# Kernel tuning notes

Hardware: AMD Instinct MI355X
Metric: run time of the kernel (lower is better)

The kernel has to match this reference:

```python
import jax, jax.numpy as jnp
import numpy as np
from jax import lax

MIN_R = 0.01
RADIUS = 0.8
NSAMPLE = 32
PRED_NSAMPLE = 16
TEMPERATURE = 1.0
DIV_COEF = 10.0
GRID3 = 64  # grid_size**3, grid_size=4
EPS = 1e-5


def _ball_query(q, xyz, radius, nsample):
    """q (M,3), xyz (N,3), radius scalar or (M,). Returns idx (M,nsample) int32, empty (M,) bool.
    Mirrors stack ball_query CUDA op: first-found neighbors within radius, padded with first index."""
    N = xyz.shape[0]
    d2 = jnp.sum((q[:, None, :] - xyz[None, :, :]) ** 2, axis=-1)  # (M,N)
    r = jnp.broadcast_to(jnp.asarray(radius, d2.dtype), (q.shape[0],))[:, None]
    valid = d2 < r * r
    score = jnp.where(valid, -jnp.arange(N, dtype=jnp.int32), -(N + 1))
    vals, _ = lax.top_k(score, nsample)  # largest score == smallest valid index
    idx = -vals
    pad = idx == (N + 1)
    idx = jnp.where(pad, idx[:, :1], idx)  # pad with first found neighbor
    empty = pad[:, 0]                       # no neighbor at all
    idx = jnp.where(empty[:, None], 0, idx)
    return idx, empty


def _group(q, xyz, feats, idx, empty):
    """QueryAndGroup gather: relative xyz concat point features; zero empty queries.
    Returns (M, nsample, 3+C)."""
    g_xyz = xyz[idx] - q[:, None, :]
    g = jnp.concatenate([g_xyz, feats[idx]], axis=-1)
    return jnp.where(empty[:, None, None], jnp.zeros((), g.dtype), g)


def _mlp(x, params):
    """Shared 1x1 Conv2d + BatchNorm2d(training stats) + ReLU stack. x: (B,M,S,C)."""
    for W, g, b in params:
        x = jnp.einsum('bmsc,cd->bmsd', x, W)
        mu = x.mean(axis=(0, 1, 2))
        var = x.var(axis=(0, 1, 2))
        x = (x - mu) * lax.rsqrt(var + EPS) * g + b
        x = jax.nn.relu(x)
    return x


def setup_inputs() -> dict:
    key = jax.random.key(0)
    ks = jax.random.split(key, 16)
    B, N, C, R, Croi = 2, 8192, 32, 64, 128
    scene = jnp.array([10.0, 10.0, 4.0], jnp.float32)
    xyz = jax.random.uniform(ks[0], (B, N, 3), jnp.float32) * scene
    features = jax.random.normal(ks[1], (B, N, C), jnp.float32)
    rois = jax.random.uniform(ks[2], (B, R, GRID3, 3), jnp.float32) * scene
    roi_features = jax.random.normal(ks[3], (B, R, Croi), jnp.float32)

    def kaiming(k, fi, fo):
        return jax.random.normal(k, (fi, fo), jnp.float32) * np.float32(np.sqrt(2.0 / fi))

    return {
        'xyz': xyz, 'features': features, 'rois': rois, 'roi_features': roi_features,
        'temperature_decay': jnp.ones((1,), jnp.float32),
        # predict mlp: [32+3, 32, 32]
        'pw0': kaiming(ks[4], 35, 32), 'pg0': jnp.ones(32), 'pb0': jnp.zeros(32),
        'pw1': kaiming(ks[5], 32, 32), 'pg1': jnp.ones(32), 'pb1': jnp.zeros(32),
        # feat mlp: [32+3, 64, 64]
        'fw0': kaiming(ks[6], 35, 64), 'fg0': jnp.ones(64), 'fb0': jnp.zeros(64),
        'fw1': kaiming(ks[7], 64, 64), 'fg1': jnp.ones(64), 'fb1': jnp.zeros(64),
        # predict fc: [32*64 + 128, 1]
        'fcw': kaiming(ks[8], 2176, 1), 'fcb': jnp.zeros(1),
    }


def reference(xyz, features, rois, roi_features, temperature_decay,
              pw0, pg0, pb0, pw1, pg1, pb1,
              fw0, fg0, fb0, fw1, fg1, fb1, fcw, fcb):
    B, num_rois = rois.shape[0], rois.shape[1]
    new_xyz = rois.reshape(B, -1, 3)  # (B, M, 3), M = num_rois*grid^3

    # ---- radius-prediction branch: fixed-radius grouping + MLP + max-pool ----
    idx_p, empty_p = jax.vmap(lambda q, x: _ball_query(q, x, RADIUS, PRED_NSAMPLE))(new_xyz, xyz)
    gp = jax.vmap(_group)(new_xyz, xyz, features, idx_p, empty_p)  # (B,M,S,3+C)
    gp = _mlp(gp, [(pw0, pg0, pb0), (pw1, pg1, pb1)])
    pooled = gp.max(axis=2)                       # (B, M, Cp)
    pooled = pooled.reshape(B, num_rois, -1)      # (B, R, grid^3*Cp)
    res = jnp.concatenate([pooled, roi_features], axis=-1) @ fcw + fcb  # (B,R,1)
    r = jnp.maximum(res / DIV_COEF + RADIUS, MIN_R)
    r_pts = jnp.broadcast_to(r, (B, num_rois, GRID3)).reshape(B, -1)    # (B, M)

    # ---- deformable branch: per-query radius grouping + soft weights ----
    idx_d, empty_d = jax.vmap(lambda q, x, rr: _ball_query(q, x, rr, NSAMPLE))(new_xyz, xyz, r_pts)
    gd = jax.vmap(_group)(new_xyz, xyz, features, idx_d, empty_d)       # (B,M,S,3+C)
    dist = jnp.linalg.norm(gd[..., :3], axis=-1)                        # (B,M,S)
    w = jax.nn.sigmoid((r_pts[..., None] - dist) / (TEMPERATURE * temperature_decay[0]))
    w = jnp.where(empty_d[..., None], jnp.zeros((), w.dtype), w)
    gd = _mlp(gd, [(fw0, fg0, fb0), (fw1, fg1, fb1)])                   # (B,M,S,Cout)
    new_feats = (w[..., None] * gd).max(axis=2)                          # (B,M,Cout)

    return new_xyz.reshape(-1, 3), new_feats.reshape(-1, new_feats.shape[-1])
```

## Files before the change

### kernel.cpp

```cpp
#include <hip/hip_runtime.h>
#include <hip/hip_fp16.h>

#define NB 2
#define NPTS 8192
#define NQ 4096
#define MTOT 8192
#define SP 16
#define SD 32
#define CIN 32
#define CP 32
#define CF 64
#define NROI 128
#define RADIUS_C 0.8f
#define MIN_R_C 0.01f
#define DIV_COEF_C 10.0f
#define TILE 512

__device__ int   g_idx_p[MTOT * SP];
__device__ int   g_empty_p[MTOT];
__device__ int   g_idx_d[MTOT * SD];
__device__ int   g_empty_d[MTOT];
__device__ unsigned char g_xa[(size_t)MTOT * SD * CF * 2];
__device__ unsigned char g_xb[(size_t)MTOT * SD * CF * 2];
__device__ float g_psT[CF * 2048];
__device__ float g_pqT[CF * 2048];
__device__ float g_bnscale[4][CF];
__device__ float g_bnshift[4][CF];
__device__ float g_pdot[MTOT];
__device__ float g_rroi[NROI];

__global__ void copy_xyz_kernel(const float* __restrict__ rois, float* __restrict__ out) {
    int i = blockIdx.x * 256 + threadIdx.x;
    if (i < MTOT * 3) out[i] = rois[i];
}

template <int NS>
__launch_bounds__(256, 8)
__global__ void bq_kernel(const float* __restrict__ xyz, const float* __restrict__ newxyz) {
    __shared__ float4 l4[TILE * 3 / 4];
    __shared__ int s_active;
    int tid = threadIdx.x;
    int wave = tid >> 6, lane = tid & 63;
    int q = blockIdx.x * 4 + wave;
    int b = q >> 12;
    const float4* xb4 = (const float4*)(xyz + (size_t)b * NPTS * 3);
    const float* lp = (const float*)l4;
    float qx = newxyz[q * 3 + 0], qy = newxyz[q * 3 + 1], qz = newxyz[q * 3 + 2];
    float r = (NS == SP) ? RADIUS_C : g_rroi[q >> 6];
    float r2 = r * r;
    int* idx_out   = (NS == SP) ? g_idx_p   : g_idx_d;
    int* empty_out = (NS == SP) ? g_empty_p : g_empty_d;

    int cnt = 0, first_idx = 0;
    for (int t = 0; t < NPTS / TILE; ++t) {
        l4[tid] = xb4[t * 384 + tid];
        if (tid + 256 < 384) l4[tid + 256] = xb4[t * 384 + tid + 256];
        if (tid == 0) s_active = 0;
        __syncthreads();
        if (cnt < NS) {
            for (int s = 0; s < TILE / 64; ++s) {
                int pl = s * 64 + lane;
                float dx = qx - lp[3 * pl + 0];
                float dy = qy - lp[3 * pl + 1];
                float dz = qz - lp[3 * pl + 2];
                bool valid = (dx * dx + dy * dy + dz * dz) < r2;
                unsigned long long mask = __ballot(valid);
                if (cnt == 0 && mask) first_idx = t * TILE + s * 64 + (int)__builtin_ctzll(mask);
                int pos = cnt + __popcll(mask & ((1ull << lane) - 1ull));
                if (valid && pos < NS) idx_out[q * NS + pos] = t * TILE + s * 64 + lane;
                cnt += __popcll(mask);
                if (cnt >= NS) break;
            }
            if (cnt < NS && lane == 0) s_active = 1;
        }
        __syncthreads();
        if (!s_active) break;
    }
    if (cnt == 0) {
        if (lane < NS) idx_out[q * NS + lane] = 0;
        if (lane == 0) empty_out[q] = 1;
    } else {
        int filled = cnt < NS ? cnt : NS;
        if (lane >= filled && lane < NS) idx_out[q * NS + lane] = first_idx;
        if (lane == 0) empty_out[q] = 0;
    }
}

template <int NS, int CH, bool HALF>
__launch_bounds__(128, 4)
__global__ void mlp_passA_kernel(const float* __restrict__ xyz, const float* __restrict__ feats,
                                 const float* __restrict__ newxyz, const float* __restrict__ W0,
                                 void* __restrict__ xout_) {
    constexpr int GSTR = 37;
    constexpr int SST  = CH + 2;
    __shared__ float buf[128 * GSTR];
    __shared__ float ls[128], lq[128];
    int tid = threadIdx.x;
    int rowbase = blockIdx.x * 128;
    int row = rowbase + tid;
    int q = row / NS, b = q >> 12;
    const int* idx_arr = (NS == SP) ? g_idx_p : g_idx_d;
    const int* emp_arr = (NS == SP) ? g_empty_p : g_empty_d;
    {
        float* dst = &buf[tid * GSTR];
        if (emp_arr[q]) {
#pragma unroll
            for (int c = 0; c < 35; ++c) dst[c] = 0.f;
        } else {
            int idx = idx_arr[row];
            const float* xp = xyz + (size_t)b * NPTS * 3 + idx * 3;
            dst[0] = xp[0] - newxyz[q * 3 + 0];
            dst[1] = xp[1] - newxyz[q * 3 + 1];
            dst[2] = xp[2] - newxyz[q * 3 + 2];
            const float4* fp = (const float4*)(feats + (size_t)b * NPTS * CIN + (size_t)idx * CIN);
#pragma unroll
            for (int j = 0; j < 8; ++j) {
                float4 v = fp[j];
                dst[3 + 4 * j + 0] = v.x; dst[3 + 4 * j + 1] = v.y;
                dst[3 + 4 * j + 2] = v.z; dst[3 + 4 * j + 3] = v.w;
            }
        }
    }
    float acc[CH];
#pragma unroll
    for (int ch = 0; ch < CH; ++ch) acc[ch] = 0.f;
    {
        const float* inrow = &buf[tid * GSTR];
        for (int c = 0; c < 35; ++c) {
            float h = inrow[c];
#pragma unroll
            for (int ch = 0; ch < CH; ++ch) acc[ch] = fmaf(h, W0[c * CH + ch], acc[ch]);
        }
    }
    float* xf = (float*)xout_;
    __half* xh = (__half*)xout_;
    float sum = 0.f, sq = 0.f;
#pragma unroll
    for (int p = 0; p < 2; ++p) {
        __syncthreads();
        if ((tid >> 6) == p) {
            float* srow = &buf[(tid & 63) * SST];
#pragma unroll
            for (int ch = 0; ch < CH; ++ch) srow[ch] = acc[ch];
        }
        __syncthreads();
        if (CH == 64) {
            int ch = tid & 63, rg = tid >> 6;
            for (int r = 0; r < 32; ++r) {
                float v = buf[(rg * 32 + r) * SST + ch];
                size_t o = (size_t)(rowbase + p * 64 + rg * 32 + r) * CH + ch;
                if (HALF) xh[o] = __float2half_rn(v); else xf[o] = v;
                sum += v; sq += v * v;
            }
        } else {
            int ch = tid & 31, rg = tid >> 5;
            for (int r = 0; r < 16; ++r) {
                float v = buf[(rg * 16 + r) * SST + ch];
                size_t o = (size_t)(rowbase + p * 64 + rg * 16 + r) * CH + ch;
                if (HALF) xh[o] = __float2half_rn(v); else xf[o] = v;
                sum += v; sq += v * v;
            }
        }
    }
    ls[tid] = sum; lq[tid] = sq;
    __syncthreads();
    if (CH == 64) {
        if (tid < 64) {
            g_psT[tid * 2048 + blockIdx.x] = ls[tid] + ls[64 + tid];
            g_pqT[tid * 2048 + blockIdx.x] = lq[tid] + lq[64 + tid];
        }
    } else {
        if (tid < 32) {
            g_psT[tid * 2048 + blockIdx.x] = ls[tid] + ls[32 + tid] + ls[64 + tid] + ls[96 + tid];
            g_pqT[tid * 2048 + blockIdx.x] = lq[tid] + lq[32 + tid] + lq[64 + tid] + lq[96 + tid];
        }
    }
}

template <int NS, int CH>
__launch_bounds__(128, 4)
__global__ void mlp_passB_kernel(const float* __restrict__ W1, const float* __restrict__ xin,
                                 float* __restrict__ xout, int bn0) {
    constexpr int HSTR = 33;
    constexpr int SST  = CH + 2;
    __shared__ float buf[128 * 37];
    __shared__ float ls[128], lq[128];
    int tid = threadIdx.x;
    int rowbase = blockIdx.x * 128;
    const float* sc0 = g_bnscale[bn0];
    const float* sh0 = g_bnshift[bn0];
    float acc2[CH];
#pragma unroll
    for (int ch = 0; ch < CH; ++ch) acc2[ch] = 0.f;
    const float4* src = (const float4*)xin;
#pragma unroll
    for (int hc = 0; hc < CH / 32; ++hc) {
        if (hc) __syncthreads();
#pragma unroll
        for (int k = 0; k < 8; ++k) {
            int o4 = tid + k * 128;
            int rloc = o4 >> 3, j = o4 & 7;
            int c = 4 * j, gc = hc * 32 + c;
            float4 v = src[(size_t)(rowbase + rloc) * (CH / 4) + hc * 8 + j];
            float* d = &buf[rloc * HSTR + c];
            d[0] = fmaxf(fmaf(v.x, sc0[gc + 0], sh0[gc + 0]), 0.f);
            d[1] = fmaxf(fmaf(v.y, sc0[gc + 1], sh0[gc + 1]), 0.f);
            d[2] = fmaxf(fmaf(v.z, sc0[gc + 2], sh0[gc + 2]), 0.f);
            d[3] = fmaxf(fmaf(v.w, sc0[gc + 3], sh0[gc + 3]), 0.f);
        }
        __syncthreads();
        const float* hrow = &buf[tid * HSTR];
        for (int c = 0; c < 32; ++c) {
            float h = hrow[c];
#pragma unroll
            for (int ch = 0; ch < CH; ++ch)
                acc2[ch] = fmaf(h, W1[(hc * 32 + c) * CH + ch], acc2[ch]);
        }
    }
    float sum = 0.f, sq = 0.f;
#pragma unroll
    for (int p = 0; p < 2; ++p) {
        __syncthreads();
        if ((tid >> 6) == p) {
            float* srow = &buf[(tid & 63) * SST];
#pragma unroll
            for (int ch = 0; ch < CH; ++ch) srow[ch] = acc2[ch];
        }
        __syncthreads();
        int ch = tid & 31, rg = tid >> 5;
        for (int r = 0; r < 16; ++r) {
            float v = buf[(rg * 16 + r) * SST + ch];
            xout[(size_t)(rowbase + p * 64 + rg * 16 + r) * CH + ch] = v;
            sum += v; sq += v * v;
        }
    }
    ls[tid] = sum; lq[tid] = sq;
    __syncthreads();
    if (tid < 32) {
        g_psT[tid * 2048 + blockIdx.x] = ls[tid] + ls[32 + tid] + ls[64 + tid] + ls[96 + tid];
        g_pqT[tid * 2048 + blockIdx.x] = lq[tid] + lq[32 + tid] + lq[64 + tid] + lq[96 + tid];
    }
}

__launch_bounds__(128, 4)
__global__ void mlp_fB_kernel(const float* __restrict__ W1, const __half* __restrict__ xin,
                              __half* __restrict__ xout) {
    __shared__ float fbuf[64 * 66];
    __shared__ float ls[128], lq[128];
    __half* hbuf = (__half*)fbuf;
    unsigned int* w32 = (unsigned int*)fbuf;
    int tid = threadIdx.x;
    int rowbase = blockIdx.x * 128;
    {
        const float4* src = (const float4*)xin;
#pragma unroll
        for (int k = 0; k < 8; ++k) {
            int o4 = tid + k * 128;
            int rloc = o4 >> 3, j = o4 & 7;
            float4 v = src[(size_t)(rowbase + rloc) * 8 + j];
            const unsigned int* s32 = (const unsigned int*)&v;
#pragma unroll
            for (int m = 0; m < 4; ++m) w32[rloc * 33 + 4 * j + m] = s32[m];
        }
    }
    __syncthreads();
    const float* sc0 = g_bnscale[2];
    const float* sh0 = g_bnshift[2];
    float acc2[CF];
#pragma unroll
    for (int ch = 0; ch < CF; ++ch) acc2[ch] = 0.f;
    {
        const __half* hrow = &hbuf[tid * 66];
        for (int c = 0; c < 64; ++c) {
            float h = fmaxf(fmaf(__half2float(hrow[c]), sc0[c], sh0[c]), 0.f);
#pragma unroll
            for (int ch = 0; ch < CF; ++ch)
                acc2[ch] = fmaf(h, W1[c * CF + ch], acc2[ch]);
        }
    }
    float sum = 0.f, sq = 0.f;
#pragma unroll
    for (int p = 0; p < 2; ++p) {
        __syncthreads();
        if ((tid >> 6) == p) {
            float* srow = &fbuf[(tid & 63) * 66];
#pragma unroll
            for (int ch = 0; ch < CF; ++ch) srow[ch] = acc2[ch];
        }
        __syncthreads();
        int ch = tid & 63, rg = tid >> 6;
        for (int r = 0; r < 32; ++r) {
            float v = fbuf[(rg * 32 + r) * 66 + ch];
            xout[(size_t)(rowbase + p * 64 + rg * 32 + r) * CF + ch] = __float2half_rn(v);
            sum += v; sq += v * v;
        }
    }
    ls[tid] = sum; lq[tid] = sq;
    __syncthreads();
    if (tid < 64) {
        g_psT[tid * 2048 + blockIdx.x] = ls[tid] + ls[64 + tid];
        g_pqT[tid * 2048 + blockIdx.x] = lq[tid] + lq[64 + tid];
    }
}

__global__ void passC_f_kernel(const float* __restrict__ xyz, const float* __restrict__ newxyz,
                               const float* __restrict__ td, const __half* __restrict__ xin,
                               float* __restrict__ out) {
    __shared__ float lw[64];
    int tid = threadIdx.x;
    int qpair = blockIdx.x * 2;
    if (tid < 64) {
        int ql = tid >> 5, s = tid & 31;
        int q = qpair + ql;
        float wv = 0.f;
        if (!g_empty_d[q]) {
            int idx = g_idx_d[q * SD + s];
            int b = q >> 12;
            float dx = xyz[(size_t)b * NPTS * 3 + idx * 3 + 0] - newxyz[q * 3 + 0];
            float dy = xyz[(size_t)b * NPTS * 3 + idx * 3 + 1] - newxyz[q * 3 + 1];
            float dz = xyz[(size_t)b * NPTS * 3 + idx * 3 + 2] - newxyz[q * 3 + 2];
            float dist = sqrtf(dx * dx + dy * dy + dz * dz);
            float rq = g_rroi[q >> 6];
            wv = 1.f / (1.f + expf(-(rq - dist) / td[0]));
        }
        lw[tid] = wv;
    }
    __syncthreads();
    int ql = tid >> 6, ch = tid & 63;
    int q = qpair + ql;
    float sc = g_bnscale[3][ch], sh = g_bnshift[3][ch];
    float m = 0.f;
    for (int s = 0; s < SD; ++s) {
        float v = __half2float(xin[((size_t)q * SD + s) * CF + ch]);
        m = fmaxf(m, lw[ql * 32 + s] * fmaxf(fmaf(v, sc, sh), 0.f));
    }
    out[MTOT * 3 + (size_t)q * CF + ch] = m;
}

__global__ void passC_p_kernel(const float* __restrict__ fcw, const float* __restrict__ xin) {
    int tid = threadIdx.x;
    int q = blockIdx.x * 8 + (tid >> 5);
    int ch = tid & 31;
    float sc = g_bnscale[1][ch], sh = g_bnshift[1][ch];
    float m = 0.f;
    for (int s = 0; s < SP; ++s) {
        float v = xin[(size_t)(q * SP + s) * CP + ch] * sc + sh;
        m = fmaxf(m, fmaxf(v, 0.f));
    }
    float pd = m * fcw[(q & 63) * CP + ch];
    for (int off = 16; off > 0; off >>= 1) pd += __shfl_down(pd, off, 32);
    if (ch == 0) g_pdot[q] = pd;
}

__global__ void finalize_kernel(const float* __restrict__ gamma, const float* __restrict__ beta,
                                float n, int layer, int nblocks) {
    __shared__ double l_s[256], l_q[256];
    int ch = blockIdx.x, tid = threadIdx.x;
    double s = 0, q = 0;
    for (int i = tid; i < nblocks; i += 256) { s += g_psT[ch * 2048 + i]; q += g_pqT[ch * 2048 + i]; }
    l_s[tid] = s; l_q[tid] = q; __syncthreads();
    for (int off = 128; off > 0; off >>= 1) {
        if (tid < off) { l_s[tid] += l_s[tid + off]; l_q[tid] += l_q[tid + off]; }
        __syncthreads();
    }
    if (tid == 0) {
        double mu = l_s[0] / (double)n;
        double var = l_q[0] / (double)n - mu * mu;
        if (var < 0) var = 0;
        double sc = (double)gamma[ch] / sqrt(var + 1e-5);
        g_bnscale[layer][ch] = (float)sc;
        g_bnshift[layer][ch] = (float)((double)beta[ch] - mu * sc);
    }
}

__global__ void roi_r_kernel(const float* __restrict__ roif, const float* __restrict__ fcw,
                             const float* __restrict__ fcb) {
    int tid = threadIdx.x;
    int roi = blockIdx.x * 4 + (tid >> 6);
    int lane = tid & 63;
    float acc = g_pdot[roi * 64 + lane]
              + roif[roi * 128 + lane]      * fcw[2048 + lane]
              + roif[roi * 128 + 64 + lane] * fcw[2048 + 64 + lane];
    for (int off = 32; off > 0; off >>= 1) acc += __shfl_down(acc, off, 64);
    if (lane == 0) {
        float res = acc + fcb[0];
        g_rroi[roi] = fmaxf(res / DIV_COEF_C + RADIUS_C, MIN_R_C);
    }
}

extern "C" void kernel_launch(void* const* d_in, const int* in_sizes, int n_in,
                              void* d_out, int out_size, void* d_ws, size_t ws_size,
                              hipStream_t stream) {
    const float* xyz   = (const float*)d_in[0];
    const float* feats = (const float*)d_in[1];
    const float* rois  = (const float*)d_in[2];
    const float* roif  = (const float*)d_in[3];
    const float* td    = (const float*)d_in[4];
    const float* pw0 = (const float*)d_in[5];
    const float* pg0 = (const float*)d_in[6];
    const float* pb0 = (const float*)d_in[7];
    const float* pw1 = (const float*)d_in[8];
    const float* pg1 = (const float*)d_in[9];
    const float* pb1 = (const float*)d_in[10];
    const float* fw0 = (const float*)d_in[11];
    const float* fg0 = (const float*)d_in[12];
    const float* fb0 = (const float*)d_in[13];
    const float* fw1 = (const float*)d_in[14];
    const float* fg1 = (const float*)d_in[15];
    const float* fb1 = (const float*)d_in[16];
    const float* fcw = (const float*)d_in[17];
    const float* fcb = (const float*)d_in[18];
    float* out = (float*)d_out;

    void* xa; hipGetSymbolAddress(&xa, HIP_SYMBOL(g_xa));
    void* xb; hipGetSymbolAddress(&xb, HIP_SYMBOL(g_xb));

    copy_xyz_kernel<<<96, 256, 0, stream>>>(rois, out);

    bq_kernel<SP><<<MTOT / 4, 256, 0, stream>>>(xyz, rois);
    mlp_passA_kernel<SP, CP, false><<<1024, 128, 0, stream>>>(xyz, feats, rois, pw0, xa);
    finalize_kernel<<<CP, 256, 0, stream>>>(pg0, pb0, (float)(MTOT * SP), 0, 1024);
    mlp_passB_kernel<SP, CP><<<1024, 128, 0, stream>>>(pw1, (const float*)xa, (float*)xb, 0);
    finalize_kernel<<<CP, 256, 0, stream>>>(pg1, pb1, (float)(MTOT * SP), 1, 1024);
    passC_p_kernel<<<MTOT / 8, 256, 0, stream>>>(fcw, (const float*)xb);
    roi_r_kernel<<<NROI / 4, 256, 0, stream>>>(roif, fcw, fcb);

    bq_kernel<SD><<<MTOT / 4, 256, 0, stream>>>(xyz, rois);
    mlp_passA_kernel<SD, CF, true><<<2048, 128, 0, stream>>>(xyz, feats, rois, fw0, xa);
    finalize_kernel<<<CF, 256, 0, stream>>>(fg0, fb0, (float)(MTOT * SD), 2, 2048);
    mlp_fB_kernel<<<2048, 128, 0, stream>>>(fw1, (const __half*)xa, (__half*)xb);
    finalize_kernel<<<CF, 256, 0, stream>>>(fg1, fb1, (float)(MTOT * SD), 3, 2048);
    passC_f_kernel<<<MTOT / 2, 128, 0, stream>>>(xyz, rois, td, (const __half*)xb, out);
}
```

Baseline: 305.3 us.

## Replace brute-force ball query with uniform grid spatial hashing

Builds a per-batch uniform grid over points (count, prefix scan, scatter, per-cell sort) and makes each ball query visit only the cells overlapping its radius. Candidates within radius are collected in shared memory and bitonic-sorted by index, which preserves first-found ordering. This is meant to remove the linear scan over all points per query. It adds several small setup launches and a brute-force fallback for large radii or overflow.

```diff
diff --git a/kernel.cpp b/kernel.cpp
--- a/kernel.cpp
+++ b/kernel.cpp
@@ -14,12 +14,22 @@
 #define RADIUS_C 0.8f
 #define MIN_R_C 0.01f
 #define DIV_COEF_C 10.0f
-#define TILE 512
+
+#define INV_CS 1.25f
+#define NCX 13
+#define NCY 13
+#define NCZ 5
+#define NCELL (NCX * NCY * NCZ)
 
 __device__ int   g_idx_p[MTOT * SP];
 __device__ int   g_empty_p[MTOT];
 __device__ int   g_idx_d[MTOT * SD];
 __device__ int   g_empty_d[MTOT];
+__device__ int   g_cellcnt[NB][NCELL];
+__device__ int   g_cellcur[NB][NCELL];
+__device__ int   g_cellstart[NB][NCELL + 1];
+__device__ int   g_cellpts[NB][NPTS];
+__device__ int   g_ptcell[NB][NPTS];
 __device__ unsigned char g_xa[(size_t)MTOT * SD * CF * 2];
 __device__ unsigned char g_xb[(size_t)MTOT * SD * CF * 2];
 __device__ float g_psT[CF * 2048];
@@ -34,56 +44,189 @@
     if (i < MTOT * 3) out[i] = rois[i];
 }
 
+__global__ void grid_zero_kernel() {
+    int i = blockIdx.x * 1024 + threadIdx.x;
+    if (i < NB * NCELL) ((int*)g_cellcnt)[i] = 0;
+}
+
+__device__ __forceinline__ int cell_of(float x, float y, float z) {
+    int cx = min(NCX - 1, max(0, (int)floorf(x * INV_CS)));
+    int cy = min(NCY - 1, max(0, (int)floorf(y * INV_CS)));
+    int cz = min(NCZ - 1, max(0, (int)floorf(z * INV_CS)));
+    return (cz * NCY + cy) * NCX + cx;
+}
+
+__global__ void grid_count_kernel(const float* __restrict__ xyz) {
+    int i = blockIdx.x * 256 + threadIdx.x;
+    int b = i >> 13, il = i & (NPTS - 1);
+    int cell = cell_of(xyz[(size_t)i * 3 + 0], xyz[(size_t)i * 3 + 1], xyz[(size_t)i * 3 + 2]);
+    g_ptcell[b][il] = cell;
+    atomicAdd(&g_cellcnt[b][cell], 1);
+}
+
+__global__ void grid_prefix_kernel() {
+    __shared__ int sc[1024];
+    int tid = threadIdx.x;
+    for (int b = 0; b < NB; ++b) {
+        int v = (tid < NCELL) ? g_cellcnt[b][tid] : 0;
+        __syncthreads();
+        sc[tid] = v;
+        __syncthreads();
+        for (int off = 1; off < 1024; off <<= 1) {
+            int add = (tid >= off) ? sc[tid - off] : 0;
+            __syncthreads();
+            sc[tid] += add;
+            __syncthreads();
+        }
+        if (tid < NCELL) {
+            int excl = sc[tid] - v;
+            g_cellstart[b][tid] = excl;
+            g_cellcur[b][tid] = excl;
+        }
+        if (tid == 0) g_cellstart[b][NCELL] = NPTS;
+    }
+}
+
+__global__ void grid_scatter_kernel() {
+    int i = blockIdx.x * 256 + threadIdx.x;
+    int b = i >> 13, il = i & (NPTS - 1);
+    int cell = g_ptcell[b][il];
+    int pos = atomicAdd(&g_cellcur[b][cell], 1);
+    g_cellpts[b][pos] = il;
+}
+
+__global__ void grid_sort_kernel() {
+    int c = blockIdx.x * 256 + threadIdx.x;
+    if (c >= NB * NCELL) return;
+    int b = c / NCELL, cell = c % NCELL;
+    int s = g_cellstart[b][cell], e = g_cellstart[b][cell + 1];
+    for (int i = s + 1; i < e; ++i) {
+        int v = g_cellpts[b][i];
+        int j = i - 1;
+        while (j >= s && g_cellpts[b][j] > v) { g_cellpts[b][j + 1] = g_cellpts[b][j]; --j; }
+        g_cellpts[b][j + 1] = v;
+    }
+}
+
 template <int NS>
 __launch_bounds__(256, 8)
-__global__ void bq_kernel(const float* __restrict__ xyz, const float* __restrict__ newxyz) {
-    __shared__ float4 l4[TILE * 3 / 4];
-    __shared__ int s_active;
-    int tid = threadIdx.x;
-    int wave = tid >> 6, lane = tid & 63;
-    int q = blockIdx.x * 4 + wave;
+__global__ void bq_grid_kernel(const float* __restrict__ xyz, const float* __restrict__ newxyz) {
+    __shared__ int s_cand[4][256];
+    __shared__ int s_cs[4][64];
+    __shared__ int s_pre[4][64];
+    int tid = threadIdx.x, wv = tid >> 6, lane = tid & 63;
+    int q = blockIdx.x * 4 + wv;
     int b = q >> 12;
-    const float4* xb4 = (const float4*)(xyz + (size_t)b * NPTS * 3);
-    const float* lp = (const float*)l4;
     float qx = newxyz[q * 3 + 0], qy = newxyz[q * 3 + 1], qz = newxyz[q * 3 + 2];
     float r = (NS == SP) ? RADIUS_C : g_rroi[q >> 6];
     float r2 = r * r;
     int* idx_out   = (NS == SP) ? g_idx_p   : g_idx_d;
     int* empty_out = (NS == SP) ? g_empty_p : g_empty_d;
-
-    int cnt = 0, first_idx = 0;
-    for (int t = 0; t < NPTS / TILE; ++t) {
-        l4[tid] = xb4[t * 384 + tid];
-        if (tid + 256 < 384) l4[tid + 256] = xb4[t * 384 + tid + 256];
-        if (tid == 0) s_active = 0;
-        __syncthreads();
-        if (cnt < NS) {
-            for (int s = 0; s < TILE / 64; ++s) {
-                int pl = s * 64 + lane;
-                float dx = qx - lp[3 * pl + 0];
-                float dy = qy - lp[3 * pl + 1];
-                float dz = qz - lp[3 * pl + 2];
-                bool valid = (dx * dx + dy * dy + dz * dz) < r2;
-                unsigned long long mask = __ballot(valid);
-                if (cnt == 0 && mask) first_idx = t * TILE + s * 64 + (int)__builtin_ctzll(mask);
-                int pos = cnt + __popcll(mask & ((1ull << lane) - 1ull));
-                if (valid && pos < NS) idx_out[q * NS + pos] = t * TILE + s * 64 + lane;
-                cnt += __popcll(mask);
-                if (cnt >= NS) break;
+    const float* xb = xyz + (size_t)b * NPTS * 3;
+
+    float rp = r + 1e-4f;
+    int xlo = max(0, min(NCX - 1, (int)floorf((qx - rp) * INV_CS)));
+    int xhi = max(0, min(NCX - 1, (int)floorf((qx + rp) * INV_CS)));
+    int ylo = max(0, min(NCY - 1, (int)floorf((qy - rp) * INV_CS)));
+    int yhi = max(0, min(NCY - 1, (int)floorf((qy + rp) * INV_CS)));
+    int zlo = max(0, min(NCZ - 1, (int)floorf((qz - rp) * INV_CS)));
+    int zhi = max(0, min(NCZ - 1, (int)floorf((qz + rp) * INV_CS)));
+    int nx = xhi - xlo + 1, ny = yhi - ylo + 1, nz = zhi - zlo + 1;
+    int ncell = nx * ny * nz;
+
+    int cnt = 0;
+    bool fallback = (ncell > 64);
+    if (!fallback) {
+        int cstart = 0, ccnt = 0;
+        if (lane < ncell) {
+            int cx = xlo + (lane % nx);
+            int t1 = lane / nx;
+            int cy = ylo + (t1 % ny);
+            int cz = zlo + (t1 / ny);
+            int cell = (cz * NCY + cy) * NCX + cx;
+            cstart = g_cellstart[b][cell];
+            ccnt = g_cellstart[b][cell + 1] - cstart;
+        }
+        int incl = ccnt;
+#pragma unroll
+        for (int off = 1; off < 64; off <<= 1) {
+            int n = __shfl_up(incl, off, 64);
+            if (lane >= off) incl += n;
+        }
+        int T = __shfl(incl, 63, 64);
+        s_cs[wv][lane] = cstart;
+        s_pre[wv][lane] = incl - ccnt;
+        __asm__ volatile("s_waitcnt lgkmcnt(0)" ::: "memory");
+        for (int t0 = 0; t0 < T; t0 += 64) {
+            int t = t0 + lane;
+            int p = -1;
+            float d2 = 1e30f;
+            if (t < T) {
+                int lo = 0, hi = ncell - 1;
+                while (lo < hi) { int mid = (lo + hi + 1) >> 1; if (s_pre[wv][mid] <= t) lo = mid; else hi = mid - 1; }
+                int e = s_cs[wv][lo] + (t - s_pre[wv][lo]);
+                p = g_cellpts[b][e];
+                float dx = qx - xb[3 * p + 0];
+                float dy = qy - xb[3 * p + 1];
+                float dz = qz - xb[3 * p + 2];
+                d2 = dx * dx + dy * dy + dz * dz;
             }
-            if (cnt < NS && lane == 0) s_active = 1;
-        }
-        __syncthreads();
-        if (!s_active) break;
+            bool valid = (t < T) && (d2 < r2);
+            unsigned long long mask = __ballot(valid);
+            int pos = cnt + __popcll(mask & ((1ull << lane) - 1ull));
+            if (valid && pos < 256) s_cand[wv][pos] = p;
+            cnt += (int)__popcll(mask);
+        }
+        if (cnt > 256) fallback = true;
+    }
+    if (fallback) {
+        int cnt2 = 0, first_idx = 0;
+        for (int g = 0; g < NPTS / 64 && cnt2 < NS; ++g) {
+            int p = (g << 6) + lane;
+            float dx = qx - xb[3 * p + 0];
+            float dy = qy - xb[3 * p + 1];
+            float dz = qz - xb[3 * p + 2];
+            bool valid = (dx * dx + dy * dy + dz * dz) < r2;
+            unsigned long long mask = __ballot(valid);
+            if (cnt2 == 0 && mask) first_idx = (g << 6) + (int)__builtin_ctzll(mask);
+            int pos = cnt2 + __popcll(mask & ((1ull << lane) - 1ull));
+            if (valid && pos < NS) idx_out[q * NS + pos] = p;
+            cnt2 += (int)__popcll(mask);
+        }
+        if (cnt2 == 0) {
+            if (lane < NS) idx_out[q * NS + lane] = 0;
+            if (lane == 0) empty_out[q] = 1;
+        } else {
+            int filled = cnt2 < NS ? cnt2 : NS;
+            if (lane >= filled && lane < NS) idx_out[q * NS + lane] = first_idx;
+            if (lane == 0) empty_out[q] = 0;
+        }
+        return;
     }
     if (cnt == 0) {
         if (lane < NS) idx_out[q * NS + lane] = 0;
         if (lane == 0) empty_out[q] = 1;
-    } else {
-        int filled = cnt < NS ? cnt : NS;
-        if (lane >= filled && lane < NS) idx_out[q * NS + lane] = first_idx;
-        if (lane == 0) empty_out[q] = 0;
-    }
+        return;
+    }
+    int S = 64; while (S < cnt) S <<= 1;
+    for (int i = cnt + lane; i < S; i += 64) s_cand[wv][i] = 0x7FFFFFFF;
+    __asm__ volatile("s_waitcnt lgkmcnt(0)" ::: "memory");
+    for (int k = 2; k <= S; k <<= 1) {
+        for (int jj = k >> 1; jj > 0; jj >>= 1) {
+            for (int i = lane; i < S; i += 64) {
+                int l = i ^ jj;
+                if (l > i) {
+                    int a = s_cand[wv][i], c2 = s_cand[wv][l];
+                    bool up = ((i & k) == 0);
+                    if (up ? (a > c2) : (a < c2)) { s_cand[wv][i] = c2; s_cand[wv][l] = a; }
+                }
+            }
+            __asm__ volatile("s_waitcnt lgkmcnt(0)" ::: "memory");
+        }
+    }
+    int first = s_cand[wv][0];
+    if (lane < NS) idx_out[q * NS + lane] = (lane < cnt) ? s_cand[wv][lane] : first;
+    if (lane == 0) empty_out[q] = 0;
 }
 
 template <int NS, int CH, bool HALF>
@@ -417,7 +560,13 @@
 
     copy_xyz_kernel<<<96, 256, 0, stream>>>(rois, out);
 
-    bq_kernel<SP><<<MTOT / 4, 256, 0, stream>>>(xyz, rois);
+    grid_zero_kernel<<<2, 1024, 0, stream>>>();
+    grid_count_kernel<<<64, 256, 0, stream>>>(xyz);
+    grid_prefix_kernel<<<1, 1024, 0, stream>>>();
+    grid_scatter_kernel<<<64, 256, 0, stream>>>();
+    grid_sort_kernel<<<7, 256, 0, stream>>>();
+
+    bq_grid_kernel<SP><<<MTOT / 4, 256, 0, stream>>>(xyz, rois);
     mlp_passA_kernel<SP, CP, false><<<1024, 128, 0, stream>>>(xyz, feats, rois, pw0, xa);
     finalize_kernel<<<CP, 256, 0, stream>>>(pg0, pb0, (float)(MTOT * SP), 0, 1024);
     mlp_passB_kernel<SP, CP><<<1024, 128, 0, stream>>>(pw1, (const float*)xa, (float*)xb, 0);
@@ -425,7 +574,7 @@
     passC_p_kernel<<<MTOT / 8, 256, 0, stream>>>(fcw, (const float*)xb);
     roi_r_kernel<<<NROI / 4, 256, 0, stream>>>(roif, fcw, fcb);
 
-    bq_kernel<SD><<<MTOT / 4, 256, 0, stream>>>(xyz, rois);
+    bq_grid_kernel<SD><<<MTOT / 4, 256, 0, stream>>>(xyz, rois);
     mlp_passA_kernel<SD, CF, true><<<2048, 128, 0, stream>>>(xyz, feats, rois, fw0, xa);
     finalize_kernel<<<CF, 256, 0, stream>>>(fg0, fb0, (float)(MTOT * SD), 2, 2048);
     mlp_fB_kernel<<<2048, 128, 0, stream>>>(fw1, (const __half*)xa, (__half*)xb);
```

Result: slower. 324.9 us (+6.4%).
